# Kernel tuning notes

Hardware: AMD Instinct MI355X
Metric: run time of the kernel (lower is better)

Reference implementation:

```python
import jax, jax.numpy as jnp
import numpy as np

N_NODES = 100000
N_EDGES = 640000
NODE_DIM = 128
EDGE_DIM = 128


def setup_inputs() -> dict:
    key = jax.random.key(0)
    ks = jax.random.split(key, 12)
    sc_n = 1.0 / np.sqrt(NODE_DIM).astype(np.float32)
    sc_e = 1.0 / np.sqrt(EDGE_DIM).astype(np.float32)
    sc_c = 1.0 / np.sqrt(2 * EDGE_DIM).astype(np.float32)
    return {
        "V": jax.random.normal(ks[0], (N_NODES, NODE_DIM), jnp.float32),
        "E": jax.random.normal(ks[1], (N_EDGES, EDGE_DIM), jnp.float32),
        "src": jax.random.randint(ks[2], (N_EDGES,), 0, N_NODES),
        "dst": jax.random.randint(ks[3], (N_EDGES,), 0, N_NODES),
        "U_w": jax.random.normal(ks[4], (EDGE_DIM, NODE_DIM), jnp.float32) * sc_n,
        "V_w": jax.random.normal(ks[5], (EDGE_DIM, NODE_DIM), jnp.float32) * sc_n,
        "P_w": jax.random.normal(ks[6], (EDGE_DIM, EDGE_DIM), jnp.float32) * sc_e,
        "P_b": jax.random.normal(ks[7], (EDGE_DIM,), jnp.float32) * sc_e,
        "W1": jax.random.normal(ks[8], (EDGE_DIM, 2 * EDGE_DIM), jnp.float32) * sc_c,
        "b1": jax.random.normal(ks[9], (EDGE_DIM,), jnp.float32) * sc_c,
        "W2": jax.random.normal(ks[10], (EDGE_DIM, EDGE_DIM), jnp.float32) * sc_e,
        "b2": jax.random.normal(ks[11], (EDGE_DIM,), jnp.float32) * sc_e,
    }


def reference(V, E, src, dst, U_w, V_w, P_w, P_b, W1, b1, W2, b2):
    # E = LeakyReLU(E)  (torch default negative_slope = 0.01)
    E_a = jax.nn.leaky_relu(E, negative_slope=0.01)  # [n_edges, edge_dim]
    # EdgePooling: P(tanh(U(V[src]) * V(V[dst])))
    h_src = jnp.einsum("en,dn->ed", V[src], U_w)      # gather + project
    h_dst = jnp.einsum("en,dn->ed", V[dst], V_w)
    pooled = jnp.tanh(h_src * h_dst) @ P_w.T + P_b    # [n_edges, edge_dim]
    # concat with edge data, then MLP (Linear+ReLU per layer)
    h = jnp.concatenate([pooled, E_a], axis=-1)       # [n_edges, 2*edge_dim]
    h = jax.nn.relu(h @ W1.T + b1)
    h = jax.nn.relu(h @ W2.T + b2)
    return h
```

## Files before the change

### kernel.cpp

```cpp
#include <hip/hip_runtime.h>

typedef __attribute__((ext_vector_type(8))) short short8;
typedef __attribute__((ext_vector_type(4))) short short4v;
typedef __attribute__((ext_vector_type(4))) float float4v;

#define N_EDGES 640000

__device__ __forceinline__ short f2bf(float f) {
  union { float f; unsigned u; } a; a.f = f;
  unsigned r = a.u + 0x7FFFu + ((a.u >> 16) & 1u);
  return (short)(r >> 16);
}

__device__ __forceinline__ float fast_tanh(float x) {
  float xc = fminf(fmaxf(x, -15.f), 15.f);
  float e = __expf(2.f * xc);
  return (e - 1.f) * __builtin_amdgcn_rcpf(e + 1.f);
}

__global__ void prep_kernel(const float* __restrict__ U_w, const float* __restrict__ V_w,
                            const float* __restrict__ P_w, const float* __restrict__ W1,
                            const float* __restrict__ W2, short* __restrict__ ws) {
  int i = blockIdx.x * 256 + threadIdx.x;
  if (i >= 98304) return;
  float v;
  if (i < 16384)       v = U_w[i];
  else if (i < 32768)  v = V_w[i - 16384];
  else if (i < 49152)  v = P_w[i - 32768];
  else if (i < 81920)  v = W1[i - 49152];
  else                 v = W2[i - 81920];
  ws[i] = f2bf(v);
}

__global__ __launch_bounds__(256, 3) void fused_kernel(
    const float* __restrict__ V, const float* __restrict__ E,
    const int* __restrict__ src, const int* __restrict__ dst,
    const short* __restrict__ wbf,
    const float* __restrict__ Pb, const float* __restrict__ b1,
    const float* __restrict__ b2, float* __restrict__ out) {
  __shared__ short bufA[64][136];
  __shared__ short bufB[64][136];
  __shared__ short bufE[64][136];

  const int tid  = threadIdx.x;
  const int lane = tid & 63;
  const int wave = tid >> 6;
  const int l15  = lane & 15;
  const int quad = lane >> 4;
  const int eb   = blockIdx.x * 64;
  const int n0   = wave * 2;

  const short* wU  = wbf;
  const short* wV  = wbf + 16384;
  const short* wP  = wbf + 32768;
  const short* wW1 = wbf + 49152;
  const short* wW2 = wbf + 81920;

  float pb[2], b1v[2], b2v[2];
#pragma unroll
  for (int n = 0; n < 2; n++) {
    int c = (n0 + n) * 16 + l15;
    pb[n] = Pb[c]; b1v[n] = b1[c]; b2v[n] = b2[c];
  }

  for (int i = tid; i < 2048; i += 256) {
    int row = i >> 5;
    int ch  = i & 31;
    int e   = eb + row;
    int s = src[e], d = dst[e];
    float4v vs = *((const float4v*)(V + (size_t)s * 128) + ch);
    float4v vd = *((const float4v*)(V + (size_t)d * 128) + ch);
    float4v ve = __builtin_nontemporal_load((const float4v*)(E + (size_t)e * 128) + ch);
    short4v ps = {f2bf(vs[0]), f2bf(vs[1]), f2bf(vs[2]), f2bf(vs[3])};
    short4v pd = {f2bf(vd[0]), f2bf(vd[1]), f2bf(vd[2]), f2bf(vd[3])};
    float e0 = ve[0] > 0.f ? ve[0] : 0.01f * ve[0];
    float e1 = ve[1] > 0.f ? ve[1] : 0.01f * ve[1];
    float e2 = ve[2] > 0.f ? ve[2] : 0.01f * ve[2];
    float e3 = ve[3] > 0.f ? ve[3] : 0.01f * ve[3];
    short4v pe = {f2bf(e0), f2bf(e1), f2bf(e2), f2bf(e3)};
    *(short4v*)&bufA[row][ch * 4] = ps;
    *(short4v*)&bufB[row][ch * 4] = pd;
    *(short4v*)&bufE[row][ch * 4] = pe;
  }
  __syncthreads();

  {
    short8 bU[2][4], bV[2][4];
#pragma unroll
    for (int n = 0; n < 2; n++)
#pragma unroll
      for (int kk = 0; kk < 4; kk++) {
        const int off = ((n0 + n) * 16 + l15) * 128 + kk * 32 + quad * 8;
        bU[n][kk] = *(const short8*)(wU + off);
        bV[n][kk] = *(const short8*)(wV + off);
      }
    float4v accS[4][2], accD[4][2];
#pragma unroll
    for (int m = 0; m < 4; m++)
#pragma unroll
      for (int n = 0; n < 2; n++) {
        accS[m][n] = (float4v){0.f, 0.f, 0.f, 0.f};
        accD[m][n] = (float4v){0.f, 0.f, 0.f, 0.f};
      }
#pragma unroll
    for (int m = 0; m < 4; m++)
#pragma unroll
      for (int kk = 0; kk < 4; kk++) {
        short8 aS = *(const short8*)&bufA[m * 16 + l15][kk * 32 + quad * 8];
        short8 aD = *(const short8*)&bufB[m * 16 + l15][kk * 32 + quad * 8];
#pragma unroll
        for (int n = 0; n < 2; n++) {
          accS[m][n] = __builtin_amdgcn_mfma_f32_16x16x32_bf16(aS, bU[n][kk], accS[m][n], 0, 0, 0);
          accD[m][n] = __builtin_amdgcn_mfma_f32_16x16x32_bf16(aD, bV[n][kk], accD[m][n], 0, 0, 0);
        }
      }
    __syncthreads();
#pragma unroll
    for (int m = 0; m < 4; m++)
#pragma unroll
      for (int n = 0; n < 2; n++)
#pragma unroll
        for (int r = 0; r < 4; r++) {
          float t = fast_tanh(accS[m][n][r] * accD[m][n][r]);
          bufA[m * 16 + quad * 4 + r][(n0 + n) * 16 + l15] = f2bf(t);
        }
  }
  __syncthreads();

  {
    short8 bP[2][4];
#pragma unroll
    for (int n = 0; n < 2; n++)
#pragma unroll
      for (int kk = 0; kk < 4; kk++)
        bP[n][kk] = *(const short8*)(wP + ((n0 + n) * 16 + l15) * 128 + kk * 32 + quad * 8);
#pragma unroll
    for (int m = 0; m < 4; m++) {
      float4v acc[2] = {(float4v){0.f,0.f,0.f,0.f}, (float4v){0.f,0.f,0.f,0.f}};
#pragma unroll
      for (int kk = 0; kk < 4; kk++) {
        short8 a = *(const short8*)&bufA[m * 16 + l15][kk * 32 + quad * 8];
#pragma unroll
        for (int n = 0; n < 2; n++)
          acc[n] = __builtin_amdgcn_mfma_f32_16x16x32_bf16(a, bP[n][kk], acc[n], 0, 0, 0);
      }
#pragma unroll
      for (int n = 0; n < 2; n++)
#pragma unroll
        for (int r = 0; r < 4; r++)
          bufB[m * 16 + quad * 4 + r][(n0 + n) * 16 + l15] = f2bf(acc[n][r] + pb[n]);
    }
  }
  __syncthreads();

  {
    short8 bW[2][8];
#pragma unroll
    for (int n = 0; n < 2; n++) {
      const int rowoff = ((n0 + n) * 16 + l15) * 256;
#pragma unroll
      for (int kk = 0; kk < 4; kk++) {
        bW[n][kk]     = *(const short8*)(wW1 + rowoff + kk * 32 + quad * 8);
        bW[n][kk + 4] = *(const short8*)(wW1 + rowoff + 128 + kk * 32 + quad * 8);
      }
    }
#pragma unroll
    for (int m = 0; m < 4; m++) {
      float4v acc[2] = {(float4v){0.f,0.f,0.f,0.f}, (float4v){0.f,0.f,0.f,0.f}};
#pragma unroll
      for (int kk = 0; kk < 4; kk++) {
        short8 a = *(const short8*)&bufB[m * 16 + l15][kk * 32 + quad * 8];
#pragma unroll
        for (int n = 0; n < 2; n++)
          acc[n] = __builtin_amdgcn_mfma_f32_16x16x32_bf16(a, bW[n][kk], acc[n], 0, 0, 0);
      }
#pragma unroll
      for (int kk = 0; kk < 4; kk++) {
        short8 a = *(const short8*)&bufE[m * 16 + l15][kk * 32 + quad * 8];
#pragma unroll
        for (int n = 0; n < 2; n++)
          acc[n] = __builtin_amdgcn_mfma_f32_16x16x32_bf16(a, bW[n][kk + 4], acc[n], 0, 0, 0);
      }
#pragma unroll
      for (int n = 0; n < 2; n++)
#pragma unroll
        for (int r = 0; r < 4; r++) {
          float v = fmaxf(acc[n][r] + b1v[n], 0.f);
          bufA[m * 16 + quad * 4 + r][(n0 + n) * 16 + l15] = f2bf(v);
        }
    }
  }
  __syncthreads();

  {
    short8 bW[2][4];
#pragma unroll
    for (int n = 0; n < 2; n++)
#pragma unroll
      for (int kk = 0; kk < 4; kk++)
        bW[n][kk] = *(const short8*)(wW2 + ((n0 + n) * 16 + l15) * 128 + kk * 32 + quad * 8);
#pragma unroll
    for (int m = 0; m < 4; m++) {
      float4v acc[2] = {(float4v){0.f,0.f,0.f,0.f}, (float4v){0.f,0.f,0.f,0.f}};
#pragma unroll
      for (int kk = 0; kk < 4; kk++) {
        short8 a = *(const short8*)&bufA[m * 16 + l15][kk * 32 + quad * 8];
#pragma unroll
        for (int n = 0; n < 2; n++)
          acc[n] = __builtin_amdgcn_mfma_f32_16x16x32_bf16(a, bW[n][kk], acc[n], 0, 0, 0);
      }
#pragma unroll
      for (int n = 0; n < 2; n++)
#pragma unroll
        for (int r = 0; r < 4; r++) {
          float v = fmaxf(acc[n][r] + b2v[n], 0.f);
          __builtin_nontemporal_store(
              v, out + (size_t)(eb + m * 16 + quad * 4 + r) * 128 + (n0 + n) * 16 + l15);
        }
    }
  }
}

extern "C" void kernel_launch(void* const* d_in, const int* in_sizes, int n_in,
                              void* d_out, int out_size, void* d_ws, size_t ws_size,
                              hipStream_t stream) {
  const float* V   = (const float*)d_in[0];
  const float* E   = (const float*)d_in[1];
  const int*   src = (const int*)d_in[2];
  const int*   dst = (const int*)d_in[3];
  const float* U_w = (const float*)d_in[4];
  const float* V_w = (const float*)d_in[5];
  const float* P_w = (const float*)d_in[6];
  const float* P_b = (const float*)d_in[7];
  const float* W1  = (const float*)d_in[8];
  const float* b1  = (const float*)d_in[9];
  const float* W2  = (const float*)d_in[10];
  const float* b2  = (const float*)d_in[11];
  short* ws = (short*)d_ws;

  hipLaunchKernelGGL(prep_kernel, dim3(384), dim3(256), 0, stream,
                     U_w, V_w, P_w, W1, W2, ws);
  hipLaunchKernelGGL(fused_kernel, dim3(N_EDGES / 64), dim3(256), 0, stream,
                     V, E, src, dst, ws, P_b, b1, b2, (float*)d_out);
}
```

Measured before the change: 829.7 us.

## Drop edge LDS buffer, hold edge features in registers, raise occupancy to 4

Removes the third shared-memory buffer by loading and activating the edge features into registers up front, then writing them into bufB after the first projection is done. The GEMM loops are restructured to be k-outer and load weight fragments per k-step instead of preloading all of them, which reduces live registers. Launch bounds rise from 3 to 4 blocks per SU. Together these aim to cut LDS and VGPR use so more waves fit and hide gather latency. The trade-off is 16 extra registers held through the first GEMM and more frequent weight reloads inside the loops.

After: 856.7 us. +3.3%, slower.

```diff
diff --git a/kernel.cpp b/kernel.cpp
--- a/kernel.cpp
+++ b/kernel.cpp
@@ -32,7 +32,7 @@
   ws[i] = f2bf(v);
 }
 
-__global__ __launch_bounds__(256, 3) void fused_kernel(
+__global__ __launch_bounds__(256, 4) void fused_kernel(
     const float* __restrict__ V, const float* __restrict__ E,
     const int* __restrict__ src, const int* __restrict__ dst,
     const short* __restrict__ wbf,
@@ -40,7 +40,6 @@
     const float* __restrict__ b2, float* __restrict__ out) {
   __shared__ short bufA[64][136];
   __shared__ short bufB[64][136];
-  __shared__ short bufE[64][136];
 
   const int tid  = threadIdx.x;
   const int lane = tid & 63;
@@ -63,6 +62,21 @@
     pb[n] = Pb[c]; b1v[n] = b1[c]; b2v[n] = b2[c];
   }
 
+  short4v eB[8];
+#pragma unroll
+  for (int i = 0; i < 8; i++) {
+    int idx = tid + (i << 8);
+    int row = idx >> 5;
+    int ch  = idx & 31;
+    float4v ve = __builtin_nontemporal_load(
+        (const float4v*)(E + (size_t)(eb + row) * 128) + ch);
+    float e0 = ve[0] > 0.f ? ve[0] : 0.01f * ve[0];
+    float e1 = ve[1] > 0.f ? ve[1] : 0.01f * ve[1];
+    float e2 = ve[2] > 0.f ? ve[2] : 0.01f * ve[2];
+    float e3 = ve[3] > 0.f ? ve[3] : 0.01f * ve[3];
+    eB[i] = (short4v){f2bf(e0), f2bf(e1), f2bf(e2), f2bf(e3)};
+  }
+
   for (int i = tid; i < 2048; i += 256) {
     int row = i >> 5;
     int ch  = i & 31;
@@ -70,154 +84,169 @@
     int s = src[e], d = dst[e];
     float4v vs = *((const float4v*)(V + (size_t)s * 128) + ch);
     float4v vd = *((const float4v*)(V + (size_t)d * 128) + ch);
-    float4v ve = __builtin_nontemporal_load((const float4v*)(E + (size_t)e * 128) + ch);
     short4v ps = {f2bf(vs[0]), f2bf(vs[1]), f2bf(vs[2]), f2bf(vs[3])};
     short4v pd = {f2bf(vd[0]), f2bf(vd[1]), f2bf(vd[2]), f2bf(vd[3])};
-    float e0 = ve[0] > 0.f ? ve[0] : 0.01f * ve[0];
-    float e1 = ve[1] > 0.f ? ve[1] : 0.01f * ve[1];
-    float e2 = ve[2] > 0.f ? ve[2] : 0.01f * ve[2];
-    float e3 = ve[3] > 0.f ? ve[3] : 0.01f * ve[3];
-    short4v pe = {f2bf(e0), f2bf(e1), f2bf(e2), f2bf(e3)};
     *(short4v*)&bufA[row][ch * 4] = ps;
     *(short4v*)&bufB[row][ch * 4] = pd;
-    *(short4v*)&bufE[row][ch * 4] = pe;
+  }
+  __syncthreads();
+
+  float4v accS[4][2], accD[4][2];
+#pragma unroll
+  for (int m = 0; m < 4; m++)
+#pragma unroll
+    for (int n = 0; n < 2; n++) {
+      accS[m][n] = (float4v){0.f, 0.f, 0.f, 0.f};
+      accD[m][n] = (float4v){0.f, 0.f, 0.f, 0.f};
+    }
+#pragma unroll
+  for (int kk = 0; kk < 4; kk++) {
+    short8 bU[2], bV[2];
+#pragma unroll
+    for (int n = 0; n < 2; n++) {
+      const int off = ((n0 + n) * 16 + l15) * 128 + kk * 32 + quad * 8;
+      bU[n] = *(const short8*)(wU + off);
+      bV[n] = *(const short8*)(wV + off);
+    }
+#pragma unroll
+    for (int m = 0; m < 4; m++) {
+      short8 aS = *(const short8*)&bufA[m * 16 + l15][kk * 32 + quad * 8];
+      short8 aD = *(const short8*)&bufB[m * 16 + l15][kk * 32 + quad * 8];
+#pragma unroll
+      for (int n = 0; n < 2; n++) {
+        accS[m][n] = __builtin_amdgcn_mfma_f32_16x16x32_bf16(aS, bU[n], accS[m][n], 0, 0, 0);
+        accD[m][n] = __builtin_amdgcn_mfma_f32_16x16x32_bf16(aD, bV[n], accD[m][n], 0, 0, 0);
+      }
+    }
+  }
+  __syncthreads();
+
+#pragma unroll
+  for (int m = 0; m < 4; m++)
+#pragma unroll
+    for (int n = 0; n < 2; n++)
+#pragma unroll
+      for (int r = 0; r < 4; r++) {
+        float t = fast_tanh(accS[m][n][r] * accD[m][n][r]);
+        bufA[m * 16 + quad * 4 + r][(n0 + n) * 16 + l15] = f2bf(t);
+      }
+#pragma unroll
+  for (int i = 0; i < 8; i++) {
+    int idx = tid + (i << 8);
+    int row = idx >> 5;
+    int ch  = idx & 31;
+    *(short4v*)&bufB[row][ch * 4] = eB[i];
   }
   __syncthreads();
 
   {
-    short8 bU[2][4], bV[2][4];
-#pragma unroll
-    for (int n = 0; n < 2; n++)
-#pragma unroll
-      for (int kk = 0; kk < 4; kk++) {
-        const int off = ((n0 + n) * 16 + l15) * 128 + kk * 32 + quad * 8;
-        bU[n][kk] = *(const short8*)(wU + off);
-        bV[n][kk] = *(const short8*)(wV + off);
-      }
-    float4v accS[4][2], accD[4][2];
-#pragma unroll
-    for (int m = 0; m < 4; m++)
-#pragma unroll
-      for (int n = 0; n < 2; n++) {
-        accS[m][n] = (float4v){0.f, 0.f, 0.f, 0.f};
-        accD[m][n] = (float4v){0.f, 0.f, 0.f, 0.f};
-      }
-#pragma unroll
-    for (int m = 0; m < 4; m++)
-#pragma unroll
-      for (int kk = 0; kk < 4; kk++) {
-        short8 aS = *(const short8*)&bufA[m * 16 + l15][kk * 32 + quad * 8];
-        short8 aD = *(const short8*)&bufB[m * 16 + l15][kk * 32 + quad * 8];
-#pragma unroll
-        for (int n = 0; n < 2; n++) {
-          accS[m][n] = __builtin_amdgcn_mfma_f32_16x16x32_bf16(aS, bU[n][kk], accS[m][n], 0, 0, 0);
-          accD[m][n] = __builtin_amdgcn_mfma_f32_16x16x32_bf16(aD, bV[n][kk], accD[m][n], 0, 0, 0);
-        }
-      }
+    float4v accP[4][2];
+#pragma unroll
+    for (int m = 0; m < 4; m++)
+#pragma unroll
+      for (int n = 0; n < 2; n++) accP[m][n] = (float4v){0.f, 0.f, 0.f, 0.f};
+#pragma unroll
+    for (int kk = 0; kk < 4; kk++) {
+      short8 bP[2];
+#pragma unroll
+      for (int n = 0; n < 2; n++)
+        bP[n] = *(const short8*)(wP + ((n0 + n) * 16 + l15) * 128 + kk * 32 + quad * 8);
+#pragma unroll
+      for (int m = 0; m < 4; m++) {
+        short8 a = *(const short8*)&bufA[m * 16 + l15][kk * 32 + quad * 8];
+#pragma unroll
+        for (int n = 0; n < 2; n++)
+          accP[m][n] = __builtin_amdgcn_mfma_f32_16x16x32_bf16(a, bP[n], accP[m][n], 0, 0, 0);
+      }
+    }
     __syncthreads();
 #pragma unroll
     for (int m = 0; m < 4; m++)
 #pragma unroll
       for (int n = 0; n < 2; n++)
 #pragma unroll
+        for (int r = 0; r < 4; r++)
+          bufA[m * 16 + quad * 4 + r][(n0 + n) * 16 + l15] = f2bf(accP[m][n][r] + pb[n]);
+  }
+  __syncthreads();
+
+  {
+    float4v accH[4][2];
+#pragma unroll
+    for (int m = 0; m < 4; m++)
+#pragma unroll
+      for (int n = 0; n < 2; n++) accH[m][n] = (float4v){0.f, 0.f, 0.f, 0.f};
+#pragma unroll
+    for (int kk = 0; kk < 4; kk++) {
+      short8 bW[2];
+#pragma unroll
+      for (int n = 0; n < 2; n++)
+        bW[n] = *(const short8*)(wW1 + ((n0 + n) * 16 + l15) * 256 + kk * 32 + quad * 8);
+#pragma unroll
+      for (int m = 0; m < 4; m++) {
+        short8 a = *(const short8*)&bufA[m * 16 + l15][kk * 32 + quad * 8];
+#pragma unroll
+        for (int n = 0; n < 2; n++)
+          accH[m][n] = __builtin_amdgcn_mfma_f32_16x16x32_bf16(a, bW[n], accH[m][n], 0, 0, 0);
+      }
+    }
+#pragma unroll
+    for (int kk = 0; kk < 4; kk++) {
+      short8 bW[2];
+#pragma unroll
+      for (int n = 0; n < 2; n++)
+        bW[n] = *(const short8*)(wW1 + ((n0 + n) * 16 + l15) * 256 + 128 + kk * 32 + quad * 8);
+#pragma unroll
+      for (int m = 0; m < 4; m++) {
+        short8 a = *(const short8*)&bufB[m * 16 + l15][kk * 32 + quad * 8];
+#pragma unroll
+        for (int n = 0; n < 2; n++)
+          accH[m][n] = __builtin_amdgcn_mfma_f32_16x16x32_bf16(a, bW[n], accH[m][n], 0, 0, 0);
+      }
+    }
+    __syncthreads();
+#pragma unroll
+    for (int m = 0; m < 4; m++)
+#pragma unroll
+      for (int n = 0; n < 2; n++)
+#pragma unroll
         for (int r = 0; r < 4; r++) {
-          float t = fast_tanh(accS[m][n][r] * accD[m][n][r]);
-          bufA[m * 16 + quad * 4 + r][(n0 + n) * 16 + l15] = f2bf(t);
-        }
-  }
-  __syncthreads();
-
-  {
-    short8 bP[2][4];
-#pragma unroll
-    for (int n = 0; n < 2; n++)
-#pragma unroll
-      for (int kk = 0; kk < 4; kk++)
-        bP[n][kk] = *(const short8*)(wP + ((n0 + n) * 16 + l15) * 128 + kk * 32 + quad * 8);
-#pragma unroll
-    for (int m = 0; m < 4; m++) {
-      float4v acc[2] = {(float4v){0.f,0.f,0.f,0.f}, (float4v){0.f,0.f,0.f,0.f}};
-#pragma unroll
-      for (int kk = 0; kk < 4; kk++) {
-        short8 a = *(const short8*)&bufA[m * 16 + l15][kk * 32 + quad * 8];
-#pragma unroll
-        for (int n = 0; n < 2; n++)
-          acc[n] = __builtin_amdgcn_mfma_f32_16x16x32_bf16(a, bP[n][kk], acc[n], 0, 0, 0);
-      }
-#pragma unroll
-      for (int n = 0; n < 2; n++)
-#pragma unroll
-        for (int r = 0; r < 4; r++)
-          bufB[m * 16 + quad * 4 + r][(n0 + n) * 16 + l15] = f2bf(acc[n][r] + pb[n]);
-    }
-  }
-  __syncthreads();
-
-  {
-    short8 bW[2][8];
-#pragma unroll
-    for (int n = 0; n < 2; n++) {
-      const int rowoff = ((n0 + n) * 16 + l15) * 256;
-#pragma unroll
-      for (int kk = 0; kk < 4; kk++) {
-        bW[n][kk]     = *(const short8*)(wW1 + rowoff + kk * 32 + quad * 8);
-        bW[n][kk + 4] = *(const short8*)(wW1 + rowoff + 128 + kk * 32 + quad * 8);
-      }
-    }
-#pragma unroll
-    for (int m = 0; m < 4; m++) {
-      float4v acc[2] = {(float4v){0.f,0.f,0.f,0.f}, (float4v){0.f,0.f,0.f,0.f}};
-#pragma unroll
-      for (int kk = 0; kk < 4; kk++) {
-        short8 a = *(const short8*)&bufB[m * 16 + l15][kk * 32 + quad * 8];
-#pragma unroll
-        for (int n = 0; n < 2; n++)
-          acc[n] = __builtin_amdgcn_mfma_f32_16x16x32_bf16(a, bW[n][kk], acc[n], 0, 0, 0);
-      }
-#pragma unroll
-      for (int kk = 0; kk < 4; kk++) {
-        short8 a = *(const short8*)&bufE[m * 16 + l15][kk * 32 + quad * 8];
-#pragma unroll
-        for (int n = 0; n < 2; n++)
-          acc[n] = __builtin_amdgcn_mfma_f32_16x16x32_bf16(a, bW[n][kk + 4], acc[n], 0, 0, 0);
-      }
-#pragma unroll
-      for (int n = 0; n < 2; n++)
-#pragma unroll
-        for (int r = 0; r < 4; r++) {
-          float v = fmaxf(acc[n][r] + b1v[n], 0.f);
+          float v = fmaxf(accH[m][n][r] + b1v[n], 0.f);
           bufA[m * 16 + quad * 4 + r][(n0 + n) * 16 + l15] = f2bf(v);
         }
-    }
   }
   __syncthreads();
 
   {
-    short8 bW[2][4];
-#pragma unroll
-    for (int n = 0; n < 2; n++)
-#pragma unroll
-      for (int kk = 0; kk < 4; kk++)
-        bW[n][kk] = *(const short8*)(wW2 + ((n0 + n) * 16 + l15) * 128 + kk * 32 + quad * 8);
-#pragma unroll
-    for (int m = 0; m < 4; m++) {
-      float4v acc[2] = {(float4v){0.f,0.f,0.f,0.f}, (float4v){0.f,0.f,0.f,0.f}};
-#pragma unroll
-      for (int kk = 0; kk < 4; kk++) {
+    float4v accO[4][2];
+#pragma unroll
+    for (int m = 0; m < 4; m++)
+#pragma unroll
+      for (int n = 0; n < 2; n++) accO[m][n] = (float4v){0.f, 0.f, 0.f, 0.f};
+#pragma unroll
+    for (int kk = 0; kk < 4; kk++) {
+      short8 bW[2];
+#pragma unroll
+      for (int n = 0; n < 2; n++)
+        bW[n] = *(const short8*)(wW2 + ((n0 + n) * 16 + l15) * 128 + kk * 32 + quad * 8);
+#pragma unroll
+      for (int m = 0; m < 4; m++) {
         short8 a = *(const short8*)&bufA[m * 16 + l15][kk * 32 + quad * 8];
 #pragma unroll
         for (int n = 0; n < 2; n++)
-          acc[n] = __builtin_amdgcn_mfma_f32_16x16x32_bf16(a, bW[n][kk], acc[n], 0, 0, 0);
-      }
+          accO[m][n] = __builtin_amdgcn_mfma_f32_16x16x32_bf16(a, bW[n], accO[m][n], 0, 0, 0);
+      }
+    }
+#pragma unroll
+    for (int m = 0; m < 4; m++)
 #pragma unroll
       for (int n = 0; n < 2; n++)
 #pragma unroll
         for (int r = 0; r < 4; r++) {
-          float v = fmaxf(acc[n][r] + b2v[n], 0.f);
+          float v = fmaxf(accO[m][n][r] + b2v[n], 0.f);
           __builtin_nontemporal_store(
               v, out + (size_t)(eb + m * 16 + quad * 4 + r) * 128 + (n0 + n) * 16 + l15);
         }
-    }
   }
 }
 
```

## Fold P projection into W1 and load edge features directly into registers

Applied to the files above, without the earlier changes.

Since pooled is linear in tanh(...), W1's first half is premultiplied by P_w on the device, and P_b is folded into b1. This removes one 128x128 GEMM stage and its LDS round trip. Edge features are now read from global memory straight into MFMA A-fragment registers instead of being staged in a third LDS buffer, and occupancy is raised to 4 blocks per CU. The fold adds one extra bf16 rounding of the fused weight, and the E loads are strided per lane rather than coalesced rows.

Result: slower. 1.071 ms (+29.1%).

```diff
diff --git a/kernel.cpp b/kernel.cpp
--- a/kernel.cpp
+++ b/kernel.cpp
@@ -18,29 +18,56 @@
   return (e - 1.f) * __builtin_amdgcn_rcpf(e + 1.f);
 }
 
-__global__ void prep_kernel(const float* __restrict__ U_w, const float* __restrict__ V_w,
-                            const float* __restrict__ P_w, const float* __restrict__ W1,
-                            const float* __restrict__ W2, short* __restrict__ ws) {
+
+__global__ void prep_cvt(const float* __restrict__ U_w, const float* __restrict__ V_w,
+                         const float* __restrict__ W1, const float* __restrict__ W2,
+                         short* __restrict__ ws) {
   int i = blockIdx.x * 256 + threadIdx.x;
-  if (i >= 98304) return;
-  float v;
-  if (i < 16384)       v = U_w[i];
-  else if (i < 32768)  v = V_w[i - 16384];
-  else if (i < 49152)  v = P_w[i - 32768];
-  else if (i < 81920)  v = W1[i - 49152];
-  else                 v = W2[i - 81920];
-  ws[i] = f2bf(v);
-}
-
-__global__ __launch_bounds__(256, 3) void fused_kernel(
+  if (i < 16384) {
+    ws[i] = f2bf(U_w[i]);
+  } else if (i < 32768) {
+    ws[i] = f2bf(V_w[i - 16384]);
+  } else if (i < 49152) {
+    int j = i - 32768;
+    ws[i + 16384] = f2bf(W1[(j >> 7) * 256 + 128 + (j & 127)]);
+  } else {
+    int j = i - 49152;
+    ws[i + 16384] = f2bf(W2[j]);
+  }
+}
+
+__global__ void prep_mm(const float* __restrict__ W1, const float* __restrict__ P_w,
+                        const float* __restrict__ P_b, const float* __restrict__ b1,
+                        short* __restrict__ ws) {
+  int i = blockIdx.x * 256 + threadIdx.x;
+  int o = i >> 7, k = i & 127;
+  const float* wrow = W1 + o * 256;
+  const float* pcol = P_w + k;
+  float a0 = 0.f, a1 = 0.f, a2 = 0.f, a3 = 0.f;
+#pragma unroll
+  for (int c = 0; c < 128; c += 4) {
+    a0 += wrow[c]     * pcol[c * 128];
+    a1 += wrow[c + 1] * pcol[(c + 1) * 128];
+    a2 += wrow[c + 2] * pcol[(c + 2) * 128];
+    a3 += wrow[c + 3] * pcol[(c + 3) * 128];
+  }
+  ws[32768 + i] = f2bf((a0 + a1) + (a2 + a3));
+  if (i < 128) {
+    const float* wr = W1 + i * 256;
+    float b = b1[i];
+    for (int c = 0; c < 128; c++) b += wr[c] * P_b[c];
+    ((float*)ws)[81920 / 2] = ((float*)ws)[81920 / 2];
+    ((float*)(ws + 81920))[i] = b;
+  }
+}
+
+__global__ __launch_bounds__(256, 4) void fused_kernel(
     const float* __restrict__ V, const float* __restrict__ E,
     const int* __restrict__ src, const int* __restrict__ dst,
     const short* __restrict__ wbf,
-    const float* __restrict__ Pb, const float* __restrict__ b1,
     const float* __restrict__ b2, float* __restrict__ out) {
   __shared__ short bufA[64][136];
   __shared__ short bufB[64][136];
-  __shared__ short bufE[64][136];
 
   const int tid  = threadIdx.x;
   const int lane = tid & 63;
@@ -50,17 +77,18 @@
   const int eb   = blockIdx.x * 64;
   const int n0   = wave * 2;
 
-  const short* wU  = wbf;
-  const short* wV  = wbf + 16384;
-  const short* wP  = wbf + 32768;
-  const short* wW1 = wbf + 49152;
-  const short* wW2 = wbf + 81920;
-
-  float pb[2], b1v[2], b2v[2];
+  const short* wU   = wbf;
+  const short* wV   = wbf + 16384;
+  const short* wM1  = wbf + 32768;
+  const short* wW1b = wbf + 49152;
+  const short* wW2  = wbf + 65536;
+  const float* b1p  = (const float*)(wbf + 81920);
+
+  float b1v[2], b2v[2];
 #pragma unroll
   for (int n = 0; n < 2; n++) {
     int c = (n0 + n) * 16 + l15;
-    pb[n] = Pb[c]; b1v[n] = b1[c]; b2v[n] = b2[c];
+    b1v[n] = b1p[c]; b2v[n] = b2[c];
   }
 
   for (int i = tid; i < 2048; i += 256) {
@@ -70,154 +98,140 @@
     int s = src[e], d = dst[e];
     float4v vs = *((const float4v*)(V + (size_t)s * 128) + ch);
     float4v vd = *((const float4v*)(V + (size_t)d * 128) + ch);
-    float4v ve = __builtin_nontemporal_load((const float4v*)(E + (size_t)e * 128) + ch);
     short4v ps = {f2bf(vs[0]), f2bf(vs[1]), f2bf(vs[2]), f2bf(vs[3])};
     short4v pd = {f2bf(vd[0]), f2bf(vd[1]), f2bf(vd[2]), f2bf(vd[3])};
-    float e0 = ve[0] > 0.f ? ve[0] : 0.01f * ve[0];
-    float e1 = ve[1] > 0.f ? ve[1] : 0.01f * ve[1];
-    float e2 = ve[2] > 0.f ? ve[2] : 0.01f * ve[2];
-    float e3 = ve[3] > 0.f ? ve[3] : 0.01f * ve[3];
-    short4v pe = {f2bf(e0), f2bf(e1), f2bf(e2), f2bf(e3)};
     *(short4v*)&bufA[row][ch * 4] = ps;
     *(short4v*)&bufB[row][ch * 4] = pd;
-    *(short4v*)&bufE[row][ch * 4] = pe;
+  }
+  __syncthreads();
+
+  float4v accS[4][2], accD[4][2];
+#pragma unroll
+  for (int m = 0; m < 4; m++)
+#pragma unroll
+    for (int n = 0; n < 2; n++) {
+      accS[m][n] = (float4v){0.f, 0.f, 0.f, 0.f};
+      accD[m][n] = (float4v){0.f, 0.f, 0.f, 0.f};
+    }
+#pragma unroll
+  for (int kk = 0; kk < 4; kk++) {
+    short8 bU[2], bV[2];
+#pragma unroll
+    for (int n = 0; n < 2; n++) {
+      const int off = ((n0 + n) * 16 + l15) * 128 + kk * 32 + quad * 8;
+      bU[n] = *(const short8*)(wU + off);
+      bV[n] = *(const short8*)(wV + off);
+    }
+#pragma unroll
+    for (int m = 0; m < 4; m++) {
+      short8 aS = *(const short8*)&bufA[m * 16 + l15][kk * 32 + quad * 8];
+      short8 aD = *(const short8*)&bufB[m * 16 + l15][kk * 32 + quad * 8];
+#pragma unroll
+      for (int n = 0; n < 2; n++) {
+        accS[m][n] = __builtin_amdgcn_mfma_f32_16x16x32_bf16(aS, bU[n], accS[m][n], 0, 0, 0);
+        accD[m][n] = __builtin_amdgcn_mfma_f32_16x16x32_bf16(aD, bV[n], accD[m][n], 0, 0, 0);
+      }
+    }
+  }
+  __syncthreads();
+
+#pragma unroll
+  for (int m = 0; m < 4; m++)
+#pragma unroll
+    for (int n = 0; n < 2; n++)
+#pragma unroll
+      for (int r = 0; r < 4; r++) {
+        float t = fast_tanh(accS[m][n][r] * accD[m][n][r]);
+        bufA[m * 16 + quad * 4 + r][(n0 + n) * 16 + l15] = f2bf(t);
+      }
+  __syncthreads();
+
+#pragma unroll
+  for (int m = 0; m < 4; m++) {
+    const float* erow = E + (size_t)(eb + m * 16 + l15) * 128;
+    float4v ef[8];
+#pragma unroll
+    for (int kk = 0; kk < 4; kk++) {
+      ef[kk * 2]     = *((const float4v*)erow + kk * 8 + quad * 2);
+      ef[kk * 2 + 1] = *((const float4v*)erow + kk * 8 + quad * 2 + 1);
+    }
+    float4v acc[2] = {(float4v){0.f,0.f,0.f,0.f}, (float4v){0.f,0.f,0.f,0.f}};
+#pragma unroll
+    for (int kk = 0; kk < 4; kk++) {
+      short8 bM[2];
+#pragma unroll
+      for (int n = 0; n < 2; n++)
+        bM[n] = *(const short8*)(wM1 + ((n0 + n) * 16 + l15) * 128 + kk * 32 + quad * 8);
+      short8 a = *(const short8*)&bufA[m * 16 + l15][kk * 32 + quad * 8];
+#pragma unroll
+      for (int n = 0; n < 2; n++)
+        acc[n] = __builtin_amdgcn_mfma_f32_16x16x32_bf16(a, bM[n], acc[n], 0, 0, 0);
+    }
+    short8 efr[4];
+#pragma unroll
+    for (int kk = 0; kk < 4; kk++) {
+      float4v x = ef[kk * 2], y = ef[kk * 2 + 1];
+      float e0 = x[0] > 0.f ? x[0] : 0.01f * x[0];
+      float e1 = x[1] > 0.f ? x[1] : 0.01f * x[1];
+      float e2 = x[2] > 0.f ? x[2] : 0.01f * x[2];
+      float e3 = x[3] > 0.f ? x[3] : 0.01f * x[3];
+      float e4 = y[0] > 0.f ? y[0] : 0.01f * y[0];
+      float e5 = y[1] > 0.f ? y[1] : 0.01f * y[1];
+      float e6 = y[2] > 0.f ? y[2] : 0.01f * y[2];
+      float e7 = y[3] > 0.f ? y[3] : 0.01f * y[3];
+      efr[kk] = (short8){f2bf(e0), f2bf(e1), f2bf(e2), f2bf(e3),
+                         f2bf(e4), f2bf(e5), f2bf(e6), f2bf(e7)};
+    }
+#pragma unroll
+    for (int kk = 0; kk < 4; kk++) {
+      short8 bW[2];
+#pragma unroll
+      for (int n = 0; n < 2; n++)
+        bW[n] = *(const short8*)(wW1b + ((n0 + n) * 16 + l15) * 128 + kk * 32 + quad * 8);
+#pragma unroll
+      for (int n = 0; n < 2; n++)
+        acc[n] = __builtin_amdgcn_mfma_f32_16x16x32_bf16(efr[kk], bW[n], acc[n], 0, 0, 0);
+    }
+#pragma unroll
+    for (int n = 0; n < 2; n++)
+#pragma unroll
+      for (int r = 0; r < 4; r++) {
+        float v = fmaxf(acc[n][r] + b1v[n], 0.f);
+        bufB[m * 16 + quad * 4 + r][(n0 + n) * 16 + l15] = f2bf(v);
+      }
   }
   __syncthreads();
 
   {
-    short8 bU[2][4], bV[2][4];
-#pragma unroll
-    for (int n = 0; n < 2; n++)
-#pragma unroll
-      for (int kk = 0; kk < 4; kk++) {
-        const int off = ((n0 + n) * 16 + l15) * 128 + kk * 32 + quad * 8;
-        bU[n][kk] = *(const short8*)(wU + off);
-        bV[n][kk] = *(const short8*)(wV + off);
-      }
-    float4v accS[4][2], accD[4][2];
+    float4v accO[4][2];
 #pragma unroll
     for (int m = 0; m < 4; m++)
 #pragma unroll
-      for (int n = 0; n < 2; n++) {
-        accS[m][n] = (float4v){0.f, 0.f, 0.f, 0.f};
-        accD[m][n] = (float4v){0.f, 0.f, 0.f, 0.f};
-      }
+      for (int n = 0; n < 2; n++) accO[m][n] = (float4v){0.f, 0.f, 0.f, 0.f};
+#pragma unroll
+    for (int kk = 0; kk < 4; kk++) {
+      short8 bW[2];
+#pragma unroll
+      for (int n = 0; n < 2; n++)
+        bW[n] = *(const short8*)(wW2 + ((n0 + n) * 16 + l15) * 128 + kk * 32 + quad * 8);
+#pragma unroll
+      for (int m = 0; m < 4; m++) {
+        short8 a = *(const short8*)&bufB[m * 16 + l15][kk * 32 + quad * 8];
+#pragma unroll
+        for (int n = 0; n < 2; n++)
+          accO[m][n] = __builtin_amdgcn_mfma_f32_16x16x32_bf16(a, bW[n], accO[m][n], 0, 0, 0);
+      }
+    }
 #pragma unroll
     for (int m = 0; m < 4; m++)
 #pragma unroll
-      for (int kk = 0; kk < 4; kk++) {
-        short8 aS = *(const short8*)&bufA[m * 16 + l15][kk * 32 + quad * 8];
-        short8 aD = *(const short8*)&bufB[m * 16 + l15][kk * 32 + quad * 8];
-#pragma unroll
-        for (int n = 0; n < 2; n++) {
-          accS[m][n] = __builtin_amdgcn_mfma_f32_16x16x32_bf16(aS, bU[n][kk], accS[m][n], 0, 0, 0);
-          accD[m][n] = __builtin_amdgcn_mfma_f32_16x16x32_bf16(aD, bV[n][kk], accD[m][n], 0, 0, 0);
-        }
-      }
-    __syncthreads();
-#pragma unroll
-    for (int m = 0; m < 4; m++)
-#pragma unroll
       for (int n = 0; n < 2; n++)
 #pragma unroll
         for (int r = 0; r < 4; r++) {
-          float t = fast_tanh(accS[m][n][r] * accD[m][n][r]);
-          bufA[m * 16 + quad * 4 + r][(n0 + n) * 16 + l15] = f2bf(t);
-        }
-  }
-  __syncthreads();
-
-  {
-    short8 bP[2][4];
-#pragma unroll
-    for (int n = 0; n < 2; n++)
-#pragma unroll
-      for (int kk = 0; kk < 4; kk++)
-        bP[n][kk] = *(const short8*)(wP + ((n0 + n) * 16 + l15) * 128 + kk * 32 + quad * 8);
-#pragma unroll
-    for (int m = 0; m < 4; m++) {
-      float4v acc[2] = {(float4v){0.f,0.f,0.f,0.f}, (float4v){0.f,0.f,0.f,0.f}};
-#pragma unroll
-      for (int kk = 0; kk < 4; kk++) {
-        short8 a = *(const short8*)&bufA[m * 16 + l15][kk * 32 + quad * 8];
-#pragma unroll
-        for (int n = 0; n < 2; n++)
-          acc[n] = __builtin_amdgcn_mfma_f32_16x16x32_bf16(a, bP[n][kk], acc[n], 0, 0, 0);
-      }
-#pragma unroll
-      for (int n = 0; n < 2; n++)
-#pragma unroll
-        for (int r = 0; r < 4; r++)
-          bufB[m * 16 + quad * 4 + r][(n0 + n) * 16 + l15] = f2bf(acc[n][r] + pb[n]);
-    }
-  }
-  __syncthreads();
-
-  {
-    short8 bW[2][8];
-#pragma unroll
-    for (int n = 0; n < 2; n++) {
-      const int rowoff = ((n0 + n) * 16 + l15) * 256;
-#pragma unroll
-      for (int kk = 0; kk < 4; kk++) {
-        bW[n][kk]     = *(const short8*)(wW1 + rowoff + kk * 32 + quad * 8);
-        bW[n][kk + 4] = *(const short8*)(wW1 + rowoff + 128 + kk * 32 + quad * 8);
-      }
-    }
-#pragma unroll
-    for (int m = 0; m < 4; m++) {
-      float4v acc[2] = {(float4v){0.f,0.f,0.f,0.f}, (float4v){0.f,0.f,0.f,0.f}};
-#pragma unroll
-      for (int kk = 0; kk < 4; kk++) {
-        short8 a = *(const short8*)&bufB[m * 16 + l15][kk * 32 + quad * 8];
-#pragma unroll
-        for (int n = 0; n < 2; n++)
-          acc[n] = __builtin_amdgcn_mfma_f32_16x16x32_bf16(a, bW[n][kk], acc[n], 0, 0, 0);
-      }
-#pragma unroll
-      for (int kk = 0; kk < 4; kk++) {
-        short8 a = *(const short8*)&bufE[m * 16 + l15][kk * 32 + quad * 8];
-#pragma unroll
-        for (int n = 0; n < 2; n++)
-          acc[n] = __builtin_amdgcn_mfma_f32_16x16x32_bf16(a, bW[n][kk + 4], acc[n], 0, 0, 0);
-      }
-#pragma unroll
-      for (int n = 0; n < 2; n++)
-#pragma unroll
-        for (int r = 0; r < 4; r++) {
-          float v = fmaxf(acc[n][r] + b1v[n], 0.f);
-          bufA[m * 16 + quad * 4 + r][(n0 + n) * 16 + l15] = f2bf(v);
-        }
-    }
-  }
-  __syncthreads();
-
-  {
-    short8 bW[2][4];
-#pragma unroll
-    for (int n = 0; n < 2; n++)
-#pragma unroll
-      for (int kk = 0; kk < 4; kk++)
-        bW[n][kk] = *(const short8*)(wW2 + ((n0 + n) * 16 + l15) * 128 + kk * 32 + quad * 8);
-#pragma unroll
-    for (int m = 0; m < 4; m++) {
-      float4v acc[2] = {(float4v){0.f,0.f,0.f,0.f}, (float4v){0.f,0.f,0.f,0.f}};
-#pragma unroll
-      for (int kk = 0; kk < 4; kk++) {
-        short8 a = *(const short8*)&bufA[m * 16 + l15][kk * 32 + quad * 8];
-#pragma unroll
-        for (int n = 0; n < 2; n++)
-          acc[n] = __builtin_amdgcn_mfma_f32_16x16x32_bf16(a, bW[n][kk], acc[n], 0, 0, 0);
-      }
-#pragma unroll
-      for (int n = 0; n < 2; n++)
-#pragma unroll
-        for (int r = 0; r < 4; r++) {
-          float v = fmaxf(acc[n][r] + b2v[n], 0.f);
+          float v = fmaxf(accO[m][n][r] + b2v[n], 0.f);
           __builtin_nontemporal_store(
               v, out + (size_t)(eb + m * 16 + quad * 4 + r) * 128 + (n0 + n) * 16 + l15);
         }
-    }
   }
 }
 
@@ -238,8 +252,8 @@
   const float* b2  = (const float*)d_in[11];
   short* ws = (short*)d_ws;
 
-  hipLaunchKernelGGL(prep_kernel, dim3(384), dim3(256), 0, stream,
-                     U_w, V_w, P_w, W1, W2, ws);
+  hipLaunchKernelGGL(prep_cvt, dim3(256), dim3(256), 0, stream, U_w, V_w, W1, W2, ws);
+  hipLaunchKernelGGL(prep_mm, dim3(64), dim3(256), 0, stream, W1, P_w, P_b, b1, ws);
   hipLaunchKernelGGL(fused_kernel, dim3(N_EDGES / 64), dim3(256), 0, stream,
-                     V, E, src, dst, ws, P_b, b1, b2, (float*)d_out);
-}
+                     V, E, src, dst, ws, b2, (float*)d_out);
+}
```
